# Kernel optimization log

Measured on AMD Instinct MI355X. Metric: run time of the kernel, lower is better.

Reference implementation:

```python
import jax, jax.numpy as jnp
import numpy as np

N, E, IN_CH, OUT_CH = 20000, 10000, 128, 64


def setup_inputs() -> dict:
    key = jax.random.key(0)
    k1, k2, k3 = jax.random.split(key, 3)
    x = jax.random.normal(k1, (N, IN_CH), dtype=jnp.float32)
    # Uniform(0,1) incidence: strictly positive degrees, same math as weighted H.
    H = jax.random.uniform(k2, (N, E), dtype=jnp.float32)
    theta = jax.random.normal(k3, (IN_CH, OUT_CH), dtype=jnp.float32) * (1.0 / np.sqrt(IN_CH))
    return {"x": x, "H": H, "theta": theta}


def reference(x, H, theta):
    # x: [N, in_ch], H: [N, E], theta: [in_ch, out_ch]
    x = x @ theta                              # [N, out_ch]
    # gen_hyedge_ft: (H @ inv(diag(colsum(H)))).T @ x == (H.T @ x) / de[:, None]
    de = jnp.sum(H, axis=0)                    # [E] hyperedge degrees
    edge_ft = (H.T @ x) / de[:, None]          # [E, out_ch]
    # gen_node_ft: inv(diag(rowsum(H))) @ H @ edge_ft == (H @ edge_ft) / dn[:, None]
    dn = jnp.sum(H, axis=1)                    # [N] node degrees
    node_ft = (H @ edge_ft) / dn[:, None]      # [N, out_ch]
    return node_ft
```

## Files before the change

### kernel.cpp

```cpp
#include <hip/hip_runtime.h>


#define N_ROWS 20000
#define E_COLS 10000
#define E_PAD  10016
#define OUT_CH 64

typedef __attribute__((ext_vector_type(4))) float f32x4;
typedef __attribute__((ext_vector_type(8))) short s16x8;

__device__ __forceinline__ unsigned short f2bf(float f) {
  unsigned int u = __float_as_uint(f);
  u += 0x7FFFu + ((u >> 16) & 1u);
  return (unsigned short)(u >> 16);
}

__global__ __launch_bounds__(256) void k1_xwt(const float* __restrict__ x,
                                              const float* __restrict__ theta,
                                              unsigned short* __restrict__ xwT) {
  __shared__ float xt[64][129];
  const int n0 = blockIdx.x * 64;
  const int t  = threadIdx.x;
  #pragma unroll
  for (int i = 0; i < 8; ++i) {
    int f  = t + 256 * i;
    int r  = f >> 5;
    int c4 = (f & 31) * 4;
    float4 v = make_float4(0.f, 0.f, 0.f, 0.f);
    if (n0 + r < N_ROWS) v = *(const float4*)&x[(long)(n0 + r) * 128 + c4];
    xt[r][c4] = v.x; xt[r][c4 + 1] = v.y; xt[r][c4 + 2] = v.z; xt[r][c4 + 3] = v.w;
  }
  __syncthreads();
  const int nl = t & 63;
  const int cg = t >> 6;
  const int n  = n0 + nl;
  float acc[16];
  #pragma unroll
  for (int i = 0; i < 16; ++i) acc[i] = 0.f;
  #pragma unroll 4
  for (int k = 0; k < 128; ++k) {
    float xv = xt[nl][k];
    const float* th = theta + k * 64 + cg * 16;
    #pragma unroll
    for (int i = 0; i < 16; ++i) acc[i] += xv * th[i];
  }
  if (n < N_ROWS) {
    #pragma unroll
    for (int i = 0; i < 16; ++i)
      xwT[(long)(cg * 16 + i) * N_ROWS + n] = f2bf(acc[i]);
  }
}

__global__ __launch_bounds__(64) void k2_edge(const float* __restrict__ H,
                                              const unsigned short* __restrict__ xwT,
                                              float* __restrict__ eacc,
                                              float* __restrict__ de) {
  const int b  = blockIdx.x;
  const int et = b % 625, s = b / 625;
  const int e0 = et * 16;
  const int l  = threadIdx.x;
  const int q  = l >> 4, eL = l & 15;
  f32x4 acc[4] = {{0,0,0,0},{0,0,0,0},{0,0,0,0},{0,0,0,0}};
  float deP = 0.f;
  const float* __restrict__ Hp = H + (e0 + eL);
  const int k0 = s * 125, k1 = k0 + 125;
  for (int kk = k0; kk < k1; ++kk) {
    const int nb = kk * 32 + q * 8;
    float v[8];
    #pragma unroll
    for (int j = 0; j < 8; ++j) v[j] = Hp[(long)(nb + j) * E_COLS];
    #pragma unroll
    for (int j = 0; j < 8; ++j) deP += v[j];
    union { s16x8 v8; unsigned short u[8]; } bf;
    #pragma unroll
    for (int j = 0; j < 8; ++j) bf.u[j] = f2bf(v[j]);
    #pragma unroll
    for (int ct = 0; ct < 4; ++ct) {
      s16x8 af = *(const s16x8*)&xwT[(long)(ct * 16 + eL) * N_ROWS + nb];
      acc[ct] = __builtin_amdgcn_mfma_f32_16x16x32_bf16(af, bf.v8, acc[ct], 0, 0, 0);
    }
  }
  #pragma unroll
  for (int ct = 0; ct < 4; ++ct)
    #pragma unroll
    for (int r = 0; r < 4; ++r) {
      int c = ct * 16 + q * 4 + r;
      atomicAdd(&eacc[(long)c * E_PAD + e0 + eL], acc[ct][r]);
    }
  deP += __shfl_xor(deP, 16, 64);
  deP += __shfl_xor(deP, 32, 64);
  if (l < 16) atomicAdd(&de[e0 + l], deP);
}

__global__ __launch_bounds__(256) void k3_edgefin(const float* __restrict__ eacc,
                                                  const float* __restrict__ de,
                                                  unsigned short* __restrict__ eT) {
  const int e = blockIdx.x * 256 + threadIdx.x;
  const int c = blockIdx.y;
  if (e >= E_PAD) return;
  float v = 0.f;
  if (e < E_COLS) v = eacc[(long)c * E_PAD + e] / de[e];
  eT[(long)c * E_PAD + e] = f2bf(v);
}

__global__ __launch_bounds__(64) void k4_node(const float* __restrict__ H,
                                              const unsigned short* __restrict__ eT,
                                              float* __restrict__ outacc,
                                              float* __restrict__ dn) {
  const int b  = blockIdx.x;
  const int mt = b % 1250, s = b / 1250;
  const int n0 = mt * 16;
  const int l  = threadIdx.x;
  const int q  = l >> 4, nL = l & 15;
  f32x4 acc[4] = {{0,0,0,0},{0,0,0,0},{0,0,0,0},{0,0,0,0}};
  float dnP = 0.f;
  const float* __restrict__ Hrow = H + (long)(n0 + nL) * E_COLS;
  const int k0 = s * 78;
  const int k1 = (s == 3) ? 313 : (k0 + 78);
  const f32x4 z4 = {0, 0, 0, 0};
  for (int kk = k0; kk < k1; ++kk) {
    const int ec = kk * 32 + q * 8;
    f32x4 v0 = (ec     < E_COLS) ? *(const f32x4*)(Hrow + ec)     : z4;
    f32x4 v1 = (ec + 4 < E_COLS) ? *(const f32x4*)(Hrow + ec + 4) : z4;
    dnP += v0[0] + v0[1] + v0[2] + v0[3] + v1[0] + v1[1] + v1[2] + v1[3];
    union { s16x8 v8; unsigned short u[8]; } af;
    #pragma unroll
    for (int j = 0; j < 4; ++j) { af.u[j] = f2bf(v0[j]); af.u[4 + j] = f2bf(v1[j]); }
    #pragma unroll
    for (int ct = 0; ct < 4; ++ct) {
      s16x8 bf = *(const s16x8*)&eT[(long)(ct * 16 + nL) * E_PAD + ec];
      acc[ct] = __builtin_amdgcn_mfma_f32_16x16x32_bf16(af.v8, bf, acc[ct], 0, 0, 0);
    }
  }
  #pragma unroll
  for (int ct = 0; ct < 4; ++ct)
    #pragma unroll
    for (int r = 0; r < 4; ++r)
      atomicAdd(&outacc[(long)(n0 + q * 4 + r) * OUT_CH + ct * 16 + nL], acc[ct][r]);
  dnP += __shfl_xor(dnP, 16, 64);
  dnP += __shfl_xor(dnP, 32, 64);
  if (l < 16) atomicAdd(&dn[n0 + l], dnP);
}

__global__ __launch_bounds__(256) void k5_nodefin(float* __restrict__ out,
                                                  const float* __restrict__ dn) {
  const int idx = blockIdx.x * 256 + threadIdx.x;
  out[idx] = out[idx] / dn[idx >> 6];
}

extern "C" void kernel_launch(void* const* d_in, const int* in_sizes, int n_in,
                              void* d_out, int out_size, void* d_ws, size_t ws_size,
                              hipStream_t stream) {
  const float* x     = (const float*)d_in[0];
  const float* H     = (const float*)d_in[1];
  const float* theta = (const float*)d_in[2];
  float* out = (float*)d_out;
  char* ws = (char*)d_ws;

  const size_t OFF_XWT  = 0;
  const size_t OFF_EACC = 2560000;
  const size_t OFF_DE   = OFF_EACC + 2564096;
  const size_t OFF_DN   = OFF_DE + 40192;
  const size_t OFF_ET   = OFF_DN + 80128;

  unsigned short* xwT = (unsigned short*)(ws + OFF_XWT);
  float*          eacc = (float*)(ws + OFF_EACC);
  float*          de   = (float*)(ws + OFF_DE);
  float*          dn   = (float*)(ws + OFF_DN);
  unsigned short* eT   = (unsigned short*)(ws + OFF_ET);

  hipMemsetAsync(eacc, 0, 2564096, stream);
  hipMemsetAsync(de,   0, 40064,   stream);
  hipMemsetAsync(dn,   0, 80000,   stream);
  hipMemsetAsync(out,  0, (size_t)out_size * sizeof(float), stream);

  k1_xwt<<<313, 256, 0, stream>>>(x, theta, xwT);
  k2_edge<<<3125, 64, 0, stream>>>(H, xwT, eacc, de);
  k3_edgefin<<<dim3(40, 64), 256, 0, stream>>>(eacc, de, eT);
  k4_node<<<5000, 64, 0, stream>>>(H, eT, out, dn);
  k5_nodefin<<<5000, 256, 0, stream>>>(out, dn);
}
```

Measured before the change: 1.526 ms.

## Stage H tiles through shared memory with coalesced loads in edge kernel

The edge-aggregation kernel previously read H column-wise with strided scalar loads (one float per row per lane). It now uses 256-thread blocks that load a 32x128 tile of H with coalesced float4 reads into LDS, register-prefetch the next tile, and feed the MFMA from LDS; xwT fragments are reused across two sub-tiles. Edge padding and split counts change accordingly, and the node kernel's split is adjusted to match the new padding. This adds LDS traffic and two barriers per step, and there are fewer K-splits per edge tile.

```diff
diff --git a/kernel.cpp b/kernel.cpp
--- a/kernel.cpp
+++ b/kernel.cpp
@@ -3,7 +3,8 @@
 
 #define N_ROWS 20000
 #define E_COLS 10000
-#define E_PAD  10016
+#define ETILE  128
+#define E_PAD2 10112
 #define OUT_CH 64
 
 typedef __attribute__((ext_vector_type(4))) float f32x4;
@@ -51,45 +52,89 @@
   }
 }
 
-__global__ __launch_bounds__(64) void k2_edge(const float* __restrict__ H,
-                                              const unsigned short* __restrict__ xwT,
-                                              float* __restrict__ eacc,
-                                              float* __restrict__ de) {
+__global__ __launch_bounds__(256) void k2_edge(const float* __restrict__ H,
+                                               const unsigned short* __restrict__ xwT,
+                                               float* __restrict__ eacc,
+                                               float* __restrict__ de) {
+  __shared__ float tile[32][ETILE + 4];
   const int b  = blockIdx.x;
-  const int et = b % 625, s = b / 625;
-  const int e0 = et * 16;
-  const int l  = threadIdx.x;
+  const int et = b % 79, s = b / 79;
+  const int e0 = et * ETILE;
+  const int t  = threadIdx.x;
+  const int w  = t >> 6;
+  const int l  = t & 63;
   const int q  = l >> 4, eL = l & 15;
-  f32x4 acc[4] = {{0,0,0,0},{0,0,0,0},{0,0,0,0},{0,0,0,0}};
-  float deP = 0.f;
-  const float* __restrict__ Hp = H + (e0 + eL);
-  const int k0 = s * 125, k1 = k0 + 125;
-  for (int kk = k0; kk < k1; ++kk) {
-    const int nb = kk * 32 + q * 8;
-    float v[8];
-    #pragma unroll
-    for (int j = 0; j < 8; ++j) v[j] = Hp[(long)(nb + j) * E_COLS];
-    #pragma unroll
-    for (int j = 0; j < 8; ++j) deP += v[j];
-    union { s16x8 v8; unsigned short u[8]; } bf;
-    #pragma unroll
-    for (int j = 0; j < 8; ++j) bf.u[j] = f2bf(v[j]);
-    #pragma unroll
-    for (int ct = 0; ct < 4; ++ct) {
-      s16x8 af = *(const s16x8*)&xwT[(long)(ct * 16 + eL) * N_ROWS + nb];
-      acc[ct] = __builtin_amdgcn_mfma_f32_16x16x32_bf16(af, bf.v8, acc[ct], 0, 0, 0);
+
+  const int sr = t >> 5;
+  const int sc = (t & 31) * 4;
+  const int eg = e0 + sc;
+  const bool egv = (eg < E_COLS);
+  const f32x4 z4 = {0, 0, 0, 0};
+
+  f32x4 acc[2][4];
+  #pragma unroll
+  for (int sub = 0; sub < 2; ++sub)
+    #pragma unroll
+    for (int ct = 0; ct < 4; ++ct) acc[sub][ct] = z4;
+  float deP[2] = {0.f, 0.f};
+
+  const int c0 = 25 * s, c1 = c0 + 25;
+
+  f32x4 pv[4];
+  #pragma unroll
+  for (int i = 0; i < 4; ++i)
+    pv[i] = egv ? *(const f32x4*)&H[(long)(c0 * 32 + sr + 8 * i) * E_COLS + eg] : z4;
+
+  for (int kk = c0; kk < c1; ++kk) {
+    const int nb = kk * 32;
+    #pragma unroll
+    for (int i = 0; i < 4; ++i)
+      *(f32x4*)&tile[sr + 8 * i][sc] = pv[i];
+    __syncthreads();
+    if (kk + 1 < c1) {
+      #pragma unroll
+      for (int i = 0; i < 4; ++i)
+        pv[i] = egv ? *(const f32x4*)&H[(long)(nb + 32 + sr + 8 * i) * E_COLS + eg] : z4;
     }
-  }
-  #pragma unroll
-  for (int ct = 0; ct < 4; ++ct)
-    #pragma unroll
-    for (int r = 0; r < 4; ++r) {
-      int c = ct * 16 + q * 4 + r;
-      atomicAdd(&eacc[(long)c * E_PAD + e0 + eL], acc[ct][r]);
+    s16x8 af[4];
+    #pragma unroll
+    for (int ct = 0; ct < 4; ++ct)
+      af[ct] = *(const s16x8*)&xwT[(long)(ct * 16 + eL) * N_ROWS + nb + 8 * q];
+    #pragma unroll
+    for (int sub = 0; sub < 2; ++sub) {
+      const int ec = 32 * w + 16 * sub + eL;
+      union { s16x8 v8; unsigned short u[8]; } bf;
+      float ds = 0.f;
+      #pragma unroll
+      for (int j = 0; j < 8; ++j) {
+        float v = tile[8 * q + j][ec];
+        ds += v;
+        bf.u[j] = f2bf(v);
+      }
+      deP[sub] += ds;
+      #pragma unroll
+      for (int ct = 0; ct < 4; ++ct)
+        acc[sub][ct] = __builtin_amdgcn_mfma_f32_16x16x32_bf16(af[ct], bf.v8, acc[sub][ct], 0, 0, 0);
     }
-  deP += __shfl_xor(deP, 16, 64);
-  deP += __shfl_xor(deP, 32, 64);
-  if (l < 16) atomicAdd(&de[e0 + l], deP);
+    __syncthreads();
+  }
+  #pragma unroll
+  for (int sub = 0; sub < 2; ++sub)
+    #pragma unroll
+    for (int ct = 0; ct < 4; ++ct)
+      #pragma unroll
+      for (int r = 0; r < 4; ++r) {
+        int c = ct * 16 + q * 4 + r;
+        int e = e0 + 32 * w + 16 * sub + eL;
+        atomicAdd(&eacc[(long)c * E_PAD2 + e], acc[sub][ct][r]);
+      }
+  #pragma unroll
+  for (int sub = 0; sub < 2; ++sub) {
+    float d = deP[sub];
+    d += __shfl_xor(d, 16, 64);
+    d += __shfl_xor(d, 32, 64);
+    if (l < 16) atomicAdd(&de[e0 + 32 * w + 16 * sub + l], d);
+  }
 }
 
 __global__ __launch_bounds__(256) void k3_edgefin(const float* __restrict__ eacc,
@@ -97,10 +142,10 @@
                                                   unsigned short* __restrict__ eT) {
   const int e = blockIdx.x * 256 + threadIdx.x;
   const int c = blockIdx.y;
-  if (e >= E_PAD) return;
+  if (e >= E_PAD2) return;
   float v = 0.f;
-  if (e < E_COLS) v = eacc[(long)c * E_PAD + e] / de[e];
-  eT[(long)c * E_PAD + e] = f2bf(v);
+  if (e < E_COLS) v = eacc[(long)c * E_PAD2 + e] / de[e];
+  eT[(long)c * E_PAD2 + e] = f2bf(v);
 }
 
 __global__ __launch_bounds__(64) void k4_node(const float* __restrict__ H,
@@ -115,8 +160,7 @@
   f32x4 acc[4] = {{0,0,0,0},{0,0,0,0},{0,0,0,0},{0,0,0,0}};
   float dnP = 0.f;
   const float* __restrict__ Hrow = H + (long)(n0 + nL) * E_COLS;
-  const int k0 = s * 78;
-  const int k1 = (s == 3) ? 313 : (k0 + 78);
+  const int k0 = s * 79, k1 = k0 + 79;
   const f32x4 z4 = {0, 0, 0, 0};
   for (int kk = k0; kk < k1; ++kk) {
     const int ec = kk * 32 + q * 8;
@@ -128,7 +172,7 @@
     for (int j = 0; j < 4; ++j) { af.u[j] = f2bf(v0[j]); af.u[4 + j] = f2bf(v1[j]); }
     #pragma unroll
     for (int ct = 0; ct < 4; ++ct) {
-      s16x8 bf = *(const s16x8*)&eT[(long)(ct * 16 + nL) * E_PAD + ec];
+      s16x8 bf = *(const s16x8*)&eT[(long)(ct * 16 + nL) * E_PAD2 + ec];
       acc[ct] = __builtin_amdgcn_mfma_f32_16x16x32_bf16(af.v8, bf, acc[ct], 0, 0, 0);
     }
   }
@@ -159,23 +203,23 @@
 
   const size_t OFF_XWT  = 0;
   const size_t OFF_EACC = 2560000;
-  const size_t OFF_DE   = OFF_EACC + 2564096;
-  const size_t OFF_DN   = OFF_DE + 40192;
+  const size_t OFF_DE   = OFF_EACC + 2588672;
+  const size_t OFF_DN   = OFF_DE + 40448;
   const size_t OFF_ET   = OFF_DN + 80128;
 
-  unsigned short* xwT = (unsigned short*)(ws + OFF_XWT);
+  unsigned short* xwT  = (unsigned short*)(ws + OFF_XWT);
   float*          eacc = (float*)(ws + OFF_EACC);
   float*          de   = (float*)(ws + OFF_DE);
   float*          dn   = (float*)(ws + OFF_DN);
   unsigned short* eT   = (unsigned short*)(ws + OFF_ET);
 
-  hipMemsetAsync(eacc, 0, 2564096, stream);
-  hipMemsetAsync(de,   0, 40064,   stream);
+  hipMemsetAsync(eacc, 0, 2588672, stream);
+  hipMemsetAsync(de,   0, 40448,   stream);
   hipMemsetAsync(dn,   0, 80000,   stream);
   hipMemsetAsync(out,  0, (size_t)out_size * sizeof(float), stream);
 
   k1_xwt<<<313, 256, 0, stream>>>(x, theta, xwT);
-  k2_edge<<<3125, 64, 0, stream>>>(H, xwT, eacc, de);
+  k2_edge<<<1975, 256, 0, stream>>>(H, xwT, eacc, de);
   k3_edgefin<<<dim3(40, 64), 256, 0, stream>>>(eacc, de, eT);
   k4_node<<<5000, 64, 0, stream>>>(H, eT, out, dn);
   k5_nodefin<<<5000, 256, 0, stream>>>(out, dn);
```

Measured after the change: 1.410 ms. 7.6% less time.
